# Optimization experiments

Hardware: AMD Instinct MI355X
Metric: run time of the kernel (lower is better)

## Reference

```python
import jax, jax.numpy as jnp
import numpy as np

K = 16                 # neighbors
CH = (64, 64, 64)      # edge-MLP channels
C_IN = 64              # input feature channels
EPS = 1e-3             # Keras BatchNormalization default epsilon


def setup_inputs() -> dict:
    key = jax.random.key(0)
    ks = jax.random.split(key, 24)
    B, N = 256, 128
    inp = {}
    inp["points"] = jax.random.normal(ks[0], (B, N, 2), jnp.float32)
    inp["features"] = jax.random.normal(ks[1], (B, N, C_IN), jnp.float32)
    ins = [2 * C_IN, CH[0], CH[1]]
    i = 2
    for l, (cin, cout) in enumerate(zip(ins, CH)):
        inp[f"w{l}"] = jax.random.normal(ks[i], (cin, cout), jnp.float32) / np.sqrt(cin).astype(np.float32); i += 1
        inp[f"g{l}"] = jnp.ones((cout,), jnp.float32)
        inp[f"b{l}"] = jnp.zeros((cout,), jnp.float32)
        inp[f"m{l}"] = 0.1 * jax.random.normal(ks[i], (cout,), jnp.float32); i += 1
        inp[f"v{l}"] = jnp.ones((cout,), jnp.float32)
    inp["wsc"] = jax.random.normal(ks[i], (C_IN, CH[-1]), jnp.float32) / np.sqrt(C_IN).astype(np.float32); i += 1
    inp["gsc"] = jnp.ones((CH[-1],), jnp.float32)
    inp["bsc"] = jnp.zeros((CH[-1],), jnp.float32)
    inp["msc"] = 0.1 * jax.random.normal(ks[i], (CH[-1],), jnp.float32)
    inp["vsc"] = jnp.ones((CH[-1],), jnp.float32)
    return inp


def _bn(x, g, b, m, v):
    # inference-mode BatchNorm over last (channel) axis
    return (x - m) * jax.lax.rsqrt(v + EPS) * g + b


def _forward(points, features, params):
    # pairwise squared distances  [B, N, N]
    r = jnp.sum(points * points, axis=-1, keepdims=True)
    d = r - 2.0 * jnp.einsum('bnd,bmd->bnm', points, points) + jnp.swapaxes(r, 1, 2)
    # k+1 nearest (incl. self), drop self  -> [B, N, K]
    _, idx = jax.lax.top_k(-d, K + 1)
    idx = idx[:, :, 1:]
    # gather neighbor features  [B, N, K, C]
    knn = jax.vmap(lambda f, i: f[i])(features, idx)
    center = features[:, :, None, :]
    # edge features: concat(center, neighbor - center)  [B, N, K, 2C]
    x = jnp.concatenate([jnp.broadcast_to(center, knn.shape), knn - center], axis=-1)
    # edge MLP: 1x1 convs == per-edge matmuls
    for (w, g, b, m, v) in params[:-1]:
        x = jax.nn.relu(_bn(jnp.einsum('bnkc,cd->bnkd', x, w), g, b, m, v))
    pooled = jnp.mean(x, axis=2)                      # [B, N, C_out]
    wsc, gsc, bsc, msc, vsc = params[-1]
    sc = _bn(features @ wsc, gsc, bsc, msc, vsc)      # shortcut 1x1 conv + BN
    return jax.nn.relu(sc + pooled)


def reference(points, features,
              w0, g0, b0, m0, v0,
              w1, g1, b1, m1, v1,
              w2, g2, b2, m2, v2,
              wsc, gsc, bsc, msc, vsc):
    params = [(w0, g0, b0, m0, v0), (w1, g1, b1, m1, v1),
              (w2, g2, b2, m2, v2), (wsc, gsc, bsc, msc, vsc)]
    return _forward(points, features, params)
```

## Files before the change

### kernel.cpp

```cpp
#include <hip/hip_runtime.h>
#include <stdint.h>


#define KK 16
#define EPSV 1e-3f
#define SW0 136
#define SW 72

typedef __bf16 bf16x8 __attribute__((ext_vector_type(8)));
typedef float f32x4 __attribute__((ext_vector_type(4)));
union B8 { uint4 u; bf16x8 v; };

__device__ __forceinline__ unsigned int f2ord(float f) {
  unsigned int u = __float_as_uint(f);
  return (u & 0x80000000u) ? ~u : (u | 0x80000000u);
}
__device__ __forceinline__ unsigned short f2bs(float f) {
  __bf16 b = (__bf16)f;
  return __builtin_bit_cast(unsigned short, b);
}
__device__ __forceinline__ unsigned int pk(float lo, float hi) {
  return (unsigned int)f2bs(lo) | ((unsigned int)f2bs(hi) << 16);
}

__global__ __launch_bounds__(256) void knn_kernel(const float* __restrict__ pts,
                                                  int* __restrict__ knn) {
  __shared__ __align__(16) unsigned long long keys[4][128];
  const int wv = threadIdx.x >> 6;
  const int lane = threadIdx.x & 63;
  const int row = blockIdx.x * 4 + wv;
  const int b = row >> 7;
  const int n = row & 127;
  const float2* pb = (const float2*)(pts + b * 128 * 2);
  const float2 pn = pb[n];
  const float rn = __fadd_rn(__fmul_rn(pn.x, pn.x), __fmul_rn(pn.y, pn.y));

  unsigned long long key0, key1;
#pragma unroll
  for (int h = 0; h < 2; ++h) {
    const int j = lane + h * 64;
    const float2 pj = pb[j];
    const float rj = __fadd_rn(__fmul_rn(pj.x, pj.x), __fmul_rn(pj.y, pj.y));
    const float dot = __fadd_rn(__fmul_rn(pn.x, pj.x), __fmul_rn(pn.y, pj.y));
    const float d = __fadd_rn(__fsub_rn(rn, __fmul_rn(2.0f, dot)), rj);
    unsigned long long k = ((unsigned long long)f2ord(d) << 32) | (unsigned int)j;
    if (h == 0) key0 = k; else key1 = k;
  }
  keys[wv][lane] = key0;
  keys[wv][lane + 64] = key1;
  int c0 = 0, c1 = 0;
#pragma unroll 8
  for (int j = 0; j < 128; j += 2) {
    const ulonglong2 kp = *(const ulonglong2*)&keys[wv][j];
    c0 += (kp.x < key0); c0 += (kp.y < key0);
    c1 += (kp.x < key1); c1 += (kp.y < key1);
  }
  const int base = (row >> 6) * 4096 + (row & 63) * KK;
  if (c0 >= 1 && c0 <= 16) knn[base + c0 - 1] = lane;
  if (c1 >= 1 && c1 <= 16) knn[base + c1 - 1] = lane + 64;
}

__global__ __launch_bounds__(256) void mlp_kernel(
    const float* __restrict__ feat, const int* knnIdx,
    const float* __restrict__ w0, const float* __restrict__ g0,
    const float* __restrict__ b0, const float* __restrict__ m0,
    const float* __restrict__ v0, const float* __restrict__ w1,
    const float* __restrict__ g1, const float* __restrict__ b1,
    const float* __restrict__ m1, const float* __restrict__ v1,
    const float* __restrict__ w2, const float* __restrict__ g2,
    const float* __restrict__ b2, const float* __restrict__ m2,
    const float* __restrict__ v2, const float* __restrict__ wsc,
    const float* __restrict__ gsc, const float* __restrict__ bsc,
    const float* __restrict__ msc, const float* __restrict__ vsc,
    float* out) {
  __shared__ __align__(16) unsigned short w0T[64 * SW0];
  __shared__ __align__(16) unsigned short w1T[64 * SW];
  __shared__ __align__(16) unsigned short w2T[64 * SW];
  __shared__ __align__(16) unsigned short wscT[64 * SW];
  __shared__ __align__(16) unsigned short X0[4][2][16 * SW];

  const int tid = threadIdx.x;
  const int wv = tid >> 6;
  const int lane = tid & 63;
  const int m = lane & 15;
  const int q4 = lane >> 4;

  const int row0 = blockIdx.x * 64 + wv * 16;
  const int kk = lane >> 2, pp = lane & 3;
  int jdx[16];
#pragma unroll
  for (int rr = 0; rr < 16; ++rr)
    jdx[rr] = knnIdx[blockIdx.x * 4096 + (wv * 16 + rr) * KK + kk];

#pragma unroll
  for (int q = 0; q < 8; ++q) {
    const int v = tid + 256 * q;
    const float4 w = ((const float4*)w0)[v];
    const int i = v >> 4, c = (v & 15) << 2;
    w0T[(c + 0) * SW0 + i] = f2bs(w.x);
    w0T[(c + 1) * SW0 + i] = f2bs(w.y);
    w0T[(c + 2) * SW0 + i] = f2bs(w.z);
    w0T[(c + 3) * SW0 + i] = f2bs(w.w);
  }
#pragma unroll
  for (int q = 0; q < 4; ++q) {
    const int v = tid + 256 * q;
    const int i = v >> 4, c = (v & 15) << 2;
    float4 w = ((const float4*)w1)[v];
    w1T[(c + 0) * SW + i] = f2bs(w.x);
    w1T[(c + 1) * SW + i] = f2bs(w.y);
    w1T[(c + 2) * SW + i] = f2bs(w.z);
    w1T[(c + 3) * SW + i] = f2bs(w.w);
    w = ((const float4*)w2)[v];
    w2T[(c + 0) * SW + i] = f2bs(w.x);
    w2T[(c + 1) * SW + i] = f2bs(w.y);
    w2T[(c + 2) * SW + i] = f2bs(w.z);
    w2T[(c + 3) * SW + i] = f2bs(w.w);
    w = ((const float4*)wsc)[v];
    wscT[(c + 0) * SW + i] = f2bs(w.x);
    wscT[(c + 1) * SW + i] = f2bs(w.y);
    wscT[(c + 2) * SW + i] = f2bs(w.z);
    wscT[(c + 3) * SW + i] = f2bs(w.w);
  }

  float s0[4], o0[4], s1[4], o1[4], s2[4], o2[4], ssc[4], osc[4];
#pragma unroll
  for (int nt = 0; nt < 4; ++nt) {
    const int c = nt * 16 + m;
    float s;
    s = g0[c] / sqrtf(v0[c] + EPSV); s0[nt] = s; o0[nt] = b0[c] - m0[c] * s;
    s = g1[c] / sqrtf(v1[c] + EPSV); s1[nt] = s; o1[nt] = b1[c] - m1[c] * s;
    s = g2[c] / sqrtf(v2[c] + EPSV); s2[nt] = s; o2[nt] = b2[c] - m2[c] * s;
    s = gsc[c] / sqrtf(vsc[c] + EPSV); ssc[nt] = s; osc[nt] = bsc[c] - msc[c] * s;
  }

  {
    const int r = lane >> 2, p = lane & 3;
    const float4* fr = (const float4*)(feat + (row0 + r) * 64);
    const float4 a = fr[p * 4 + 0], bq = fr[p * 4 + 1];
    const float4 cq = fr[p * 4 + 2], dq = fr[p * 4 + 3];
    uint4 u0, u1;
    u0.x = pk(a.x, a.y); u0.y = pk(a.z, a.w);
    u0.z = pk(bq.x, bq.y); u0.w = pk(bq.z, bq.w);
    u1.x = pk(cq.x, cq.y); u1.y = pk(cq.z, cq.w);
    u1.z = pk(dq.x, dq.y); u1.w = pk(dq.z, dq.w);
    *(uint4*)&X0[wv][0][r * SW + p * 16] = u0;
    *(uint4*)&X0[wv][0][r * SW + p * 16 + 8] = u1;
  }

  const float* featb = feat + (row0 >> 7) * (128 * 64);

  uint4 uA0, uA1, uB0, uB1;
  {
    const float4* np_ = (const float4*)(featb + jdx[0] * 64);
    const float4 n0 = np_[pp * 4 + 0], n1 = np_[pp * 4 + 1];
    const float4 n2 = np_[pp * 4 + 2], n3 = np_[pp * 4 + 3];
    uA0.x = pk(n0.x, n0.y); uA0.y = pk(n0.z, n0.w);
    uA0.z = pk(n1.x, n1.y); uA0.w = pk(n1.z, n1.w);
    uA1.x = pk(n2.x, n2.y); uA1.y = pk(n2.z, n2.w);
    uA1.z = pk(n3.x, n3.y); uA1.w = pk(n3.z, n3.w);
  }
  {
    const float4* np_ = (const float4*)(featb + jdx[1] * 64);
    const float4 n0 = np_[pp * 4 + 0], n1 = np_[pp * 4 + 1];
    const float4 n2 = np_[pp * 4 + 2], n3 = np_[pp * 4 + 3];
    uB0.x = pk(n0.x, n0.y); uB0.y = pk(n0.z, n0.w);
    uB0.z = pk(n1.x, n1.y); uB0.w = pk(n1.z, n1.w);
    uB1.x = pk(n2.x, n2.y); uB1.y = pk(n2.z, n2.w);
    uB1.z = pk(n3.x, n3.y); uB1.w = pk(n3.z, n3.w);
  }

  __syncthreads();

  const f32x4 fzero = {0.f, 0.f, 0.f, 0.f};
  f32x4 sacc[4] = {fzero, fzero, fzero, fzero};
  f32x4 ctp[4] = {fzero, fzero, fzero, fzero};
  f32x4 cbt[4] = {fzero, fzero, fzero, fzero};
#pragma unroll
  for (int t = 0; t < 2; ++t) {
    B8 af; af.u = *(const uint4*)&X0[wv][0][m * SW + t * 32 + q4 * 8];
#pragma unroll
    for (int nt = 0; nt < 4; ++nt) {
      B8 bs, bt, bb;
      bs.u = *(const uint4*)&wscT[(nt * 16 + m) * SW + t * 32 + q4 * 8];
      bt.u = *(const uint4*)&w0T[(nt * 16 + m) * SW0 + t * 32 + q4 * 8];
      bb.u = *(const uint4*)&w0T[(nt * 16 + m) * SW0 + 64 + t * 32 + q4 * 8];
      sacc[nt] = __builtin_amdgcn_mfma_f32_16x16x32_bf16(af.v, bs.v, sacc[nt], 0, 0, 0);
      ctp[nt]  = __builtin_amdgcn_mfma_f32_16x16x32_bf16(af.v, bt.v, ctp[nt], 0, 0, 0);
      cbt[nt]  = __builtin_amdgcn_mfma_f32_16x16x32_bf16(af.v, bb.v, cbt[nt], 0, 0, 0);
    }
  }
  float scf[4][4], ct[4][4];
#pragma unroll
  for (int nt = 0; nt < 4; ++nt)
#pragma unroll
    for (int r = 0; r < 4; ++r) {
      scf[nt][r] = fmaf(sacc[nt][r], ssc[nt], osc[nt]);
      ct[nt][r] = ctp[nt][r] - cbt[nt][r];
    }

#pragma unroll
  for (int rp = 0; rp < 8; ++rp) {
    const int qo = rp >> 1;
    const int riA = (2 * rp) & 3, riB = (2 * rp + 1) & 3;
    const int rowA = row0 + 2 * rp, rowB = rowA + 1;

    *(uint4*)&X0[wv][0][kk * SW + pp * 16] = uA0;
    *(uint4*)&X0[wv][0][kk * SW + pp * 16 + 8] = uA1;
    *(uint4*)&X0[wv][1][kk * SW + pp * 16] = uB0;
    *(uint4*)&X0[wv][1][kk * SW + pp * 16 + 8] = uB1;

    if (rp < 7) {
      {
        const float4* np_ = (const float4*)(featb + jdx[2 * rp + 2] * 64);
        const float4 n0 = np_[pp * 4 + 0], n1 = np_[pp * 4 + 1];
        const float4 n2 = np_[pp * 4 + 2], n3 = np_[pp * 4 + 3];
        uA0.x = pk(n0.x, n0.y); uA0.y = pk(n0.z, n0.w);
        uA0.z = pk(n1.x, n1.y); uA0.w = pk(n1.z, n1.w);
        uA1.x = pk(n2.x, n2.y); uA1.y = pk(n2.z, n2.w);
        uA1.z = pk(n3.x, n3.y); uA1.w = pk(n3.z, n3.w);
      }
      {
        const float4* np_ = (const float4*)(featb + jdx[2 * rp + 3] * 64);
        const float4 n0 = np_[pp * 4 + 0], n1 = np_[pp * 4 + 1];
        const float4 n2 = np_[pp * 4 + 2], n3 = np_[pp * 4 + 3];
        uB0.x = pk(n0.x, n0.y); uB0.y = pk(n0.z, n0.w);
        uB0.z = pk(n1.x, n1.y); uB0.w = pk(n1.z, n1.w);
        uB1.x = pk(n2.x, n2.y); uB1.y = pk(n2.z, n2.w);
        uB1.z = pk(n3.x, n3.y); uB1.w = pk(n3.z, n3.w);
      }
    }

    f32x4 accA[4], accB[4];
#pragma unroll
    for (int nt = 0; nt < 4; ++nt) {
      const float cA = __shfl(ct[nt][riA], qo * 16 + m);
      const float cB = __shfl(ct[nt][riB], qo * 16 + m);
      f32x4 a; a[0] = cA; a[1] = cA; a[2] = cA; a[3] = cA;
      accA[nt] = a;
      f32x4 b; b[0] = cB; b[1] = cB; b[2] = cB; b[3] = cB;
      accB[nt] = b;
    }
#pragma unroll
    for (int t = 0; t < 2; ++t) {
      B8 afA, afB;
      afA.u = *(const uint4*)&X0[wv][0][m * SW + t * 32 + q4 * 8];
      afB.u = *(const uint4*)&X0[wv][1][m * SW + t * 32 + q4 * 8];
#pragma unroll
      for (int nt = 0; nt < 4; ++nt) {
        B8 bf_; bf_.u = *(const uint4*)&w0T[(nt * 16 + m) * SW0 + 64 + t * 32 + q4 * 8];
        accA[nt] = __builtin_amdgcn_mfma_f32_16x16x32_bf16(afA.v, bf_.v, accA[nt], 0, 0, 0);
        accB[nt] = __builtin_amdgcn_mfma_f32_16x16x32_bf16(afB.v, bf_.v, accB[nt], 0, 0, 0);
      }
    }
#pragma unroll
    for (int nt = 0; nt < 4; ++nt)
#pragma unroll
      for (int r2 = 0; r2 < 4; ++r2) {
        const float yA = fmaxf(fmaf(accA[nt][r2], s0[nt], o0[nt]), 0.f);
        const float yB = fmaxf(fmaf(accB[nt][r2], s0[nt], o0[nt]), 0.f);
        X0[wv][0][(q4 * 4 + r2) * SW + nt * 16 + m] = f2bs(yA);
        X0[wv][1][(q4 * 4 + r2) * SW + nt * 16 + m] = f2bs(yB);
      }

#pragma unroll
    for (int nt = 0; nt < 4; ++nt) { accA[nt] = fzero; accB[nt] = fzero; }
#pragma unroll
    for (int t = 0; t < 2; ++t) {
      B8 afA, afB;
      afA.u = *(const uint4*)&X0[wv][0][m * SW + t * 32 + q4 * 8];
      afB.u = *(const uint4*)&X0[wv][1][m * SW + t * 32 + q4 * 8];
#pragma unroll
      for (int nt = 0; nt < 4; ++nt) {
        B8 bf_; bf_.u = *(const uint4*)&w1T[(nt * 16 + m) * SW + t * 32 + q4 * 8];
        accA[nt] = __builtin_amdgcn_mfma_f32_16x16x32_bf16(afA.v, bf_.v, accA[nt], 0, 0, 0);
        accB[nt] = __builtin_amdgcn_mfma_f32_16x16x32_bf16(afB.v, bf_.v, accB[nt], 0, 0, 0);
      }
    }
#pragma unroll
    for (int nt = 0; nt < 4; ++nt)
#pragma unroll
      for (int r2 = 0; r2 < 4; ++r2) {
        const float yA = fmaxf(fmaf(accA[nt][r2], s1[nt], o1[nt]), 0.f);
        const float yB = fmaxf(fmaf(accB[nt][r2], s1[nt], o1[nt]), 0.f);
        X0[wv][0][(q4 * 4 + r2) * SW + nt * 16 + m] = f2bs(yA);
        X0[wv][1][(q4 * 4 + r2) * SW + nt * 16 + m] = f2bs(yB);
      }

#pragma unroll
    for (int nt = 0; nt < 4; ++nt) { accA[nt] = fzero; accB[nt] = fzero; }
#pragma unroll
    for (int t = 0; t < 2; ++t) {
      B8 afA, afB;
      afA.u = *(const uint4*)&X0[wv][0][m * SW + t * 32 + q4 * 8];
      afB.u = *(const uint4*)&X0[wv][1][m * SW + t * 32 + q4 * 8];
#pragma unroll
      for (int nt = 0; nt < 4; ++nt) {
        B8 bf_; bf_.u = *(const uint4*)&w2T[(nt * 16 + m) * SW + t * 32 + q4 * 8];
        accA[nt] = __builtin_amdgcn_mfma_f32_16x16x32_bf16(afA.v, bf_.v, accA[nt], 0, 0, 0);
        accB[nt] = __builtin_amdgcn_mfma_f32_16x16x32_bf16(afB.v, bf_.v, accB[nt], 0, 0, 0);
      }
    }

    float poolA[4], poolB[4];
#pragma unroll
    for (int nt = 0; nt < 4; ++nt) {
      float pa = 0.f, pb2 = 0.f;
#pragma unroll
      for (int r2 = 0; r2 < 4; ++r2) {
        pa += fmaxf(fmaf(accA[nt][r2], s2[nt], o2[nt]), 0.f);
        pb2 += fmaxf(fmaf(accB[nt][r2], s2[nt], o2[nt]), 0.f);
      }
      pa += __shfl_xor(pa, 16);
      pa += __shfl_xor(pa, 32);
      poolA[nt] = pa * 0.0625f;
      pb2 += __shfl_xor(pb2, 16);
      pb2 += __shfl_xor(pb2, 32);
      poolB[nt] = pb2 * 0.0625f;
    }
    if (q4 == qo) {
#pragma unroll
      for (int nt = 0; nt < 4; ++nt) {
        out[rowA * 64 + nt * 16 + m] = fmaxf(scf[nt][riA] + poolA[nt], 0.f);
        out[rowB * 64 + nt * 16 + m] = fmaxf(scf[nt][riB] + poolB[nt], 0.f);
      }
    }
  }
}

extern "C" void kernel_launch(void* const* d_in, const int* in_sizes, int n_in,
                              void* d_out, int out_size, void* d_ws, size_t ws_size,
                              hipStream_t stream) {
  const float* pts = (const float*)d_in[0];
  const float* feat = (const float*)d_in[1];
  const float* w0 = (const float*)d_in[2];
  const float* g0 = (const float*)d_in[3];
  const float* b0 = (const float*)d_in[4];
  const float* m0 = (const float*)d_in[5];
  const float* v0 = (const float*)d_in[6];
  const float* w1 = (const float*)d_in[7];
  const float* g1 = (const float*)d_in[8];
  const float* b1 = (const float*)d_in[9];
  const float* m1 = (const float*)d_in[10];
  const float* v1 = (const float*)d_in[11];
  const float* w2 = (const float*)d_in[12];
  const float* g2 = (const float*)d_in[13];
  const float* b2 = (const float*)d_in[14];
  const float* m2 = (const float*)d_in[15];
  const float* v2 = (const float*)d_in[16];
  const float* wsc = (const float*)d_in[17];
  const float* gsc = (const float*)d_in[18];
  const float* bsc = (const float*)d_in[19];
  const float* msc = (const float*)d_in[20];
  const float* vsc = (const float*)d_in[21];
  float* out = (float*)d_out;

  (void)d_ws; (void)ws_size;

  int* knn = (int*)d_out;

  knn_kernel<<<dim3(256 * 128 / 4), dim3(256), 0, stream>>>(pts, knn);
  mlp_kernel<<<dim3(512), dim3(256), 0, stream>>>(
      feat, knn, w0, g0, b0, m0, v0, w1, g1, b1, m1, v1, w2, g2, b2, m2, v2,
      wsc, gsc, bsc, msc, vsc, out);
}
```

Baseline: 170.5 us.

## Process eight query rows per wave in kNN kernel with shared point staging

Each wave in the kNN kernel now handles eight query points instead of one, and the grid shrinks from 8192 blocks to 1024. The batch's 128 points are loaded once into shared memory per block, and the per-column squared norms are computed once per wave. This cuts launch and block-scheduling overhead and redundant global loads. The cost is serialized per-row work inside each wave, plus explicit LDS wait fences around the key buffer that is reused across rows.

Result: no change. 172.9 us (+1.4%).

```diff
diff --git a/kernel.cpp b/kernel.cpp
--- a/kernel.cpp
+++ b/kernel.cpp
@@ -7,6 +7,12 @@
 #define SW0 136
 #define SW 72
 
+#define LDS_FENCE()                                     \
+  do {                                                  \
+    asm volatile("s_waitcnt lgkmcnt(0)" ::: "memory");  \
+    __builtin_amdgcn_sched_barrier(0);                  \
+  } while (0)
+
 typedef __bf16 bf16x8 __attribute__((ext_vector_type(8)));
 typedef float f32x4 __attribute__((ext_vector_type(4)));
 union B8 { uint4 u; bf16x8 v; };
@@ -26,38 +32,52 @@
 __global__ __launch_bounds__(256) void knn_kernel(const float* __restrict__ pts,
                                                   int* __restrict__ knn) {
   __shared__ __align__(16) unsigned long long keys[4][128];
-  const int wv = threadIdx.x >> 6;
-  const int lane = threadIdx.x & 63;
-  const int row = blockIdx.x * 4 + wv;
-  const int b = row >> 7;
-  const int n = row & 127;
-  const float2* pb = (const float2*)(pts + b * 128 * 2);
-  const float2 pn = pb[n];
-  const float rn = __fadd_rn(__fmul_rn(pn.x, pn.x), __fmul_rn(pn.y, pn.y));
-
-  unsigned long long key0, key1;
-#pragma unroll
-  for (int h = 0; h < 2; ++h) {
-    const int j = lane + h * 64;
-    const float2 pj = pb[j];
-    const float rj = __fadd_rn(__fmul_rn(pj.x, pj.x), __fmul_rn(pj.y, pj.y));
-    const float dot = __fadd_rn(__fmul_rn(pn.x, pj.x), __fmul_rn(pn.y, pj.y));
-    const float d = __fadd_rn(__fsub_rn(rn, __fmul_rn(2.0f, dot)), rj);
-    unsigned long long k = ((unsigned long long)f2ord(d) << 32) | (unsigned int)j;
-    if (h == 0) key0 = k; else key1 = k;
-  }
-  keys[wv][lane] = key0;
-  keys[wv][lane + 64] = key1;
-  int c0 = 0, c1 = 0;
+  __shared__ __align__(16) float2 pts_s[128];
+  const int tid = threadIdx.x;
+  const int wv = tid >> 6;
+  const int lane = tid & 63;
+  const int b = blockIdx.x >> 2;
+  const int nbase = (blockIdx.x & 3) * 32 + wv * 8;
+
+  if (tid < 64) {
+    const float4 p4 = ((const float4*)(pts + b * 256))[tid];
+    *(float4*)&pts_s[2 * tid] = p4;
+  }
+  __syncthreads();
+
+  const float2 pj0 = pts_s[lane];
+  const float2 pj1 = pts_s[lane + 64];
+  const float rj0 = __fadd_rn(__fmul_rn(pj0.x, pj0.x), __fmul_rn(pj0.y, pj0.y));
+  const float rj1 = __fadd_rn(__fmul_rn(pj1.x, pj1.x), __fmul_rn(pj1.y, pj1.y));
+
+  for (int r = 0; r < 8; ++r) {
+    const int n = nbase + r;
+    const float2 pn = pts_s[n];
+    const float rn = __fadd_rn(__fmul_rn(pn.x, pn.x), __fmul_rn(pn.y, pn.y));
+    const float dot0 = __fadd_rn(__fmul_rn(pn.x, pj0.x), __fmul_rn(pn.y, pj0.y));
+    const float dot1 = __fadd_rn(__fmul_rn(pn.x, pj1.x), __fmul_rn(pn.y, pj1.y));
+    const float d0 = __fadd_rn(__fsub_rn(rn, __fmul_rn(2.0f, dot0)), rj0);
+    const float d1 = __fadd_rn(__fsub_rn(rn, __fmul_rn(2.0f, dot1)), rj1);
+    const unsigned long long key0 =
+        ((unsigned long long)f2ord(d0) << 32) | (unsigned int)lane;
+    const unsigned long long key1 =
+        ((unsigned long long)f2ord(d1) << 32) | (unsigned int)(lane + 64);
+    LDS_FENCE();
+    keys[wv][lane] = key0;
+    keys[wv][lane + 64] = key1;
+    LDS_FENCE();
+    int c0 = 0, c1 = 0;
 #pragma unroll 8
-  for (int j = 0; j < 128; j += 2) {
-    const ulonglong2 kp = *(const ulonglong2*)&keys[wv][j];
-    c0 += (kp.x < key0); c0 += (kp.y < key0);
-    c1 += (kp.x < key1); c1 += (kp.y < key1);
-  }
-  const int base = (row >> 6) * 4096 + (row & 63) * KK;
-  if (c0 >= 1 && c0 <= 16) knn[base + c0 - 1] = lane;
-  if (c1 >= 1 && c1 <= 16) knn[base + c1 - 1] = lane + 64;
+    for (int j = 0; j < 128; j += 2) {
+      const ulonglong2 kp = *(const ulonglong2*)&keys[wv][j];
+      c0 += (kp.x < key0); c0 += (kp.y < key0);
+      c1 += (kp.x < key1); c1 += (kp.y < key1);
+    }
+    const int row = b * 128 + n;
+    const int base = (row >> 6) * 4096 + (row & 63) * KK;
+    if (c0 >= 1 && c0 <= 16) knn[base + c0 - 1] = lane;
+    if (c1 >= 1 && c1 <= 16) knn[base + c1 - 1] = lane + 64;
+  }
 }
 
 __global__ __launch_bounds__(256) void mlp_kernel(
@@ -359,7 +379,7 @@
 
   int* knn = (int*)d_out;
 
-  knn_kernel<<<dim3(256 * 128 / 4), dim3(256), 0, stream>>>(pts, knn);
+  knn_kernel<<<dim3(1024), dim3(256), 0, stream>>>(pts, knn);
   mlp_kernel<<<dim3(512), dim3(256), 0, stream>>>(
       feat, knn, w0, g0, b0, m0, v0, w1, g1, b1, m1, v1, w2, g2, b2, m2, v2,
       wsc, gsc, bsc, msc, vsc, out);
```
